# Optimization experiments

Measured on AMD Instinct MI355X. Metric: run time of the kernel, lower is better.

## Reference

```python
import jax, jax.numpy as jnp
import numpy as np
from jax import lax

# Module hyperparameters (match init_kwargs)
N_EXPERTS = 8
TOP_K = 2
N_CLUSTERS = 64
TEMP = 1.0
BETA = 0.9        # LIF membrane decay
VTH = 1.0         # LIF firing threshold
SURR_ALPHA = 4.0  # surrogate-gradient sharpness


@jax.custom_vjp
def spike(u):
    # Heaviside spike with sigmoid surrogate gradient (standard SNN practice)
    return (u >= 0).astype(u.dtype)

def _spike_fwd(u):
    return spike(u), u

def _spike_bwd(u, g):
    s = jax.nn.sigmoid(SURR_ALPHA * u)
    return (g * SURR_ALPHA * s * (1.0 - s),)

spike.defvjp(_spike_fwd, _spike_bwd)


def lif(x):
    """LIF neuron over leading time axis. x: (T, ...). Returns spikes (T, ...)."""
    def step(v, xt):
        v = BETA * v + xt
        s = spike(v - VTH)
        return v - s * VTH, s  # soft reset
    _, spikes = lax.scan(step, jnp.zeros_like(x[0]), x)
    return spikes


def setup_inputs() -> dict:
    key = jax.random.key(0)
    k1, k2, k3 = jax.random.split(key, 3)
    T, B, S, D = 4, 2, 1024, 1024
    ef = 4096 // N_EXPERTS  # 512
    x = jax.random.normal(k1, (T, B, S, D), dtype=jnp.float32)
    w_up = jax.random.normal(k2, (N_EXPERTS, D, ef), dtype=jnp.float32) / np.sqrt(D)
    w_down = jax.random.normal(k3, (N_EXPERTS, ef, D), dtype=jnp.float32) / np.sqrt(ef)
    expert_bias = jnp.zeros((N_EXPERTS,), dtype=jnp.float32)
    return {"x": x, "w_up": w_up, "w_down": w_down, "expert_bias": expert_bias}


def reference(x, w_up, w_down, expert_bias):
    T, B, S, D = x.shape
    N = B * S
    xf = x.reshape(T, N, D)

    # --- routing: LIF spikes -> cluster firing rates -> expert scores ---
    rs = lif(xf)                      # (T, N, D)
    fr = rs.mean(axis=0)              # (N, D) mean firing rate
    nc = N_CLUSTERS
    # feature d belongs to cluster d % nc -> reshape(N, D//nc, nc) sums same residues
    cr = fr.reshape(N, D // nc, nc).sum(axis=1) / (D // nc)       # (N, nc)
    cpe = nc // N_EXPERTS
    es = cr.reshape(N, N_EXPERTS, cpe).mean(axis=-1)              # (N, E)
    es = es / max(TEMP, 0.01) + expert_bias

    # --- top-k expert selection ---
    ts, ti = lax.top_k(es, TOP_K)                                 # (N, k)
    tw = jax.nn.softmax(ts, axis=-1).astype(x.dtype)              # (N, k)
    # combined per-(token, expert) weight: sum_k 1[ti==e] * tw
    w = (jax.nn.one_hot(ti, N_EXPERTS, dtype=x.dtype) * tw[..., None]).sum(axis=1)  # (N, E)

    # --- expert FFN with LIF nonlinearities (all experts, masked combine) ---
    # LIF is independent per (token, feature), so computing every expert on every
    # token and weighting by w (zero for unselected) matches the masked dispatch.
    h = jnp.einsum('tnd,edf->tenf', xf, w_up)                     # (T, E, N, ef)
    hs = lif(h)
    o = jnp.einsum('tenf,efd->tend', hs, w_down)                  # (T, E, N, D)
    os = lif(o)
    out = jnp.einsum('tend,ne->tnd', os, w).reshape(T, B, S, D)

    # --- load balance loss ---
    ef_frac = jax.nn.one_hot(ti, N_EXPERTS, dtype=jnp.float32).sum(axis=(0, 1)) / (N * TOP_K)
    rp = jax.nn.softmax(es, axis=-1).mean(axis=0)
    lb = N_EXPERTS * (ef_frac * rp).sum()
    return out, lb
```

## Files before the change

### kernel.cpp

```cpp
#include <hip/hip_runtime.h>
#include <cstdint>
#include <cstddef>

#define T_   4
#define NTOK 2048
#define D_   1024
#define EF   512
#define NE   8
#define TP   8

typedef __attribute__((ext_vector_type(4))) double d4;

#define WS_RP    0
#define WS_CNT   131072
#define WS_LTOK  131104
#define WS_LW    196640
#define WS_GMASK 327712

__global__ __launch_bounds__(256) void moe_routing(
    const float* __restrict__ x, const float* __restrict__ bias,
    double* __restrict__ rp, int* __restrict__ cnt,
    int* __restrict__ ltok, double* __restrict__ lw)
{
    const int n   = blockIdx.x;
    const int tid = threadIdx.x;
    __shared__ int scnt[NE];
    if (tid < NE) scnt[tid] = 0;
    __syncthreads();

    int c = 0;
#pragma unroll
    for (int j = 0; j < 4; ++j) {
        const int d = j * 256 + tid;
        double v = 0.0;
#pragma unroll
        for (int t = 0; t < T_; ++t) {
            v = 0.9 * v + (double)x[((size_t)t * NTOK + n) * D_ + d];
            if (v - 1.0 >= 0.0) { ++c; v -= 1.0; }
        }
    }
    c += __shfl_xor(c, 1);
    c += __shfl_xor(c, 2);
    c += __shfl_xor(c, 4);
    if ((tid & 7) == 0) atomicAdd(&scnt[(tid >> 3) & 7], c);
    __syncthreads();

    if (tid == 0) {
        double es[NE];
#pragma unroll
        for (int e = 0; e < NE; ++e)
            es[e] = (double)scnt[e] * (1.0 / 512.0) + (double)bias[e];

        int i0 = 0; double b0 = es[0];
        for (int e = 1; e < NE; ++e) if (es[e] > b0) { b0 = es[e]; i0 = e; }
        int i1 = -1; double b1 = -1e300;
        for (int e = 0; e < NE; ++e) if (e != i0 && es[e] > b1) { b1 = es[e]; i1 = e; }

        const double e1 = exp(b1 - b0);
        const double w0 = 1.0 / (1.0 + e1);
        const double w1 = e1 / (1.0 + e1);

        double mx = es[0];
        for (int e = 1; e < NE; ++e) mx = es[e] > mx ? es[e] : mx;
        double s = 0.0, ex[NE];
        for (int e = 0; e < NE; ++e) { ex[e] = exp(es[e] - mx); s += ex[e]; }
        for (int e = 0; e < NE; ++e) rp[(size_t)n * NE + e] = ex[e] / s;

        int s0 = atomicAdd(&cnt[i0], 1);
        ltok[i0 * NTOK + s0] = n; lw[i0 * NTOK + s0] = w0;
        int s1 = atomicAdd(&cnt[i1], 1);
        ltok[i1 * NTOK + s1] = n; lw[i1 * NTOK + s1] = w1;
    }
}

__global__ __launch_bounds__(256) void moe_finalize(
    const double* __restrict__ rp, const int* __restrict__ cnt,
    float* __restrict__ out_lb)
{
    __shared__ double red[256][NE];
    const int tid = threadIdx.x;
    double a[NE];
#pragma unroll
    for (int e = 0; e < NE; ++e) a[e] = 0.0;
    for (int n = tid; n < NTOK; n += 256)
#pragma unroll
        for (int e = 0; e < NE; ++e) a[e] += rp[(size_t)n * NE + e];
#pragma unroll
    for (int e = 0; e < NE; ++e) red[tid][e] = a[e];
    __syncthreads();
    if (tid < NE) {
        double s = 0.0;
        for (int i = 0; i < 256; ++i) s += red[i][tid];
        red[0][tid] = s;
    }
    __syncthreads();
    if (tid == 0) {
        double lb = 0.0;
#pragma unroll
        for (int e = 0; e < NE; ++e)
            lb += ((double)cnt[e] / (double)(NTOK * 2)) * (red[0][e] / (double)NTOK);
        out_lb[0] = (float)(8.0 * lb);
    }
}

__device__ __forceinline__ int dec_idx(double val, int* fam) {
    const double r0 = (val - 96.0) * 0.25;
    const int i0 = (int)r0;
    if ((double)i0 == r0 && i0 >= 0 && i0 < 16) { *fam = 0; return i0; }
    const double r1 = (val - 6.0) * 0.0625;
    const int i1 = (int)r1;
    if ((double)i1 == r1 && i1 >= 0 && i1 < 16) { *fam = 1; return i1; }
    *fam = -1; return 0;
}

struct Frag {
    int vA, kA, uB, kB;
    int vC[4], uC[4];
    int bad;
};

__device__ __forceinline__ Frag probe_layout(int l) {
    Frag fr; fr.bad = 0;
    const d4 zz = {0.0, 0.0, 0.0, 0.0};
    const double dl = (double)l;
    const d4 Dv = __builtin_amdgcn_mfma_f64_16x16x4f64(dl, 1.0, zz, 0, 0, 0);
    const d4 Du = __builtin_amdgcn_mfma_f64_16x16x4f64(1.0, dl, zz, 0, 0, 0);
    int famA = -1, famB = -1;
#pragma unroll
    for (int r = 0; r < 4; ++r) {
        int fa, fb;
        fr.vC[r] = dec_idx(Dv[r], &fa);
        fr.uC[r] = dec_idx(Du[r], &fb);
        if (r == 0) { famA = fa; famB = fb; }
        fr.bad |= (fa != famA) | (fb != famB) | (fa < 0) | (fb < 0);
    }
    fr.vA = (famA == 0) ? (l & 15) : (l >> 2);
    fr.kA = (famA == 0) ? (l >> 4) : (l & 3);
    fr.uB = (famB == 0) ? (l & 15) : (l >> 2);
    fr.kB = (famB == 0) ? (l >> 4) : (l & 3);
    const d4 D3 = __builtin_amdgcn_mfma_f64_16x16x4f64(
        (double)(1 << fr.kA), (double)(16 << fr.kB), zz, 0, 0, 0);
#pragma unroll
    for (int r = 0; r < 4; ++r) fr.bad |= (D3[r] != 1360.0);
    return fr;
}

__device__ __forceinline__ size_t gm_row(int e, int pairIdx, int t) {
    return ((size_t)((e << 11) + pairIdx) * 4 + t) * 32;
}

__global__ __launch_bounds__(256) void moe_up(
    const float* __restrict__ x, const float* __restrict__ wup,
    const int* __restrict__ cnt, const int* __restrict__ ltok,
    unsigned short* __restrict__ gmask)
{
    const int gid  = blockIdx.x;
    const int e    = gid & 7;
    const int tile = gid >> 3;
    const int c    = cnt[e];
    const int base = tile * TP;
    if (base >= c) return;

    const int tid = threadIdx.x;
    const int w   = tid >> 6;
    const int l   = tid & 63;

    __shared__ int    s_tok[TP];
    __shared__ double dtile[4][16][17];
    __shared__ int s_bad;

    if (tid < TP) {
        const int idx = base + tid;
        s_tok[tid] = (idx < c) ? ltok[e * NTOK + idx] : ltok[e * NTOK + base];
    }
    if (tid == 0) s_bad = 0;
    __syncthreads();

    const Frag fr = probe_layout(l);
    if (fr.bad) atomicOr(&s_bad, 1);
    __syncthreads();

    if (s_bad) {
        unsigned* gm32 = (unsigned*)gmask;
        for (int i = tid; i < TP * 4 * 16; i += 256) {
            const int pr = i >> 6;
            gm32[(gm_row(e, base + pr, (i >> 4) & 3) >> 1) + (i & 15)] = 0u;
        }
        __syncthreads();
        for (int ci = tid; ci < TP * EF; ci += 256) {
            const int pair = ci >> 9;
            const int f    = ci & (EF - 1);
            const float* wc = wup + (size_t)e * D_ * EF + f;
            const float* xb = x + (size_t)s_tok[pair] * D_;
            double hh[4] = {0.0, 0.0, 0.0, 0.0};
            for (int d = 0; d < D_; ++d) {
                const double wv = (double)wc[(size_t)d * EF];
#pragma unroll
                for (int t = 0; t < 4; ++t)
                    hh[t] = fma((double)xb[(size_t)t * NTOK * D_ + d], wv, hh[t]);
            }
            double v = 0.0;
#pragma unroll
            for (int t = 0; t < 4; ++t) {
                v = 0.9 * v + hh[t];
                if (v - 1.0 >= 0.0) {
                    v -= 1.0;
                    atomicOr(&gm32[(gm_row(e, base + pair, t) >> 1) + (f >> 5)],
                             1u << (f & 31));
                }
            }
        }
        return;
    }

    const float* xp0 = x + ((size_t)(fr.vA & 3) * NTOK + s_tok[fr.vA >> 2]) * D_ + fr.kA;
    const float* xp1 = x + ((size_t)(fr.vA & 3) * NTOK + s_tok[4 + (fr.vA >> 2)]) * D_ + fr.kA;
    const float* bp  = wup + (size_t)e * D_ * EF + (size_t)fr.kB * EF + w * 128 + fr.uB;

    const d4 zz = {0.0, 0.0, 0.0, 0.0};
    d4 acc0[8], acc1[8];
#pragma unroll
    for (int j = 0; j < 8; ++j) { acc0[j] = zz; acc1[j] = zz; }

#pragma unroll 4
    for (int kk = 0; kk < 256; ++kk) {
        const double aD0 = (double)xp0[0];
        const double aD1 = (double)xp1[0];
        float b[8];
#pragma unroll
        for (int j = 0; j < 8; ++j) b[j] = bp[j * 16];
#pragma unroll
        for (int j = 0; j < 8; ++j) {
            const double bD = (double)b[j];
            acc0[j] = __builtin_amdgcn_mfma_f64_16x16x4f64(aD0, bD, acc0[j], 0, 0, 0);
            acc1[j] = __builtin_amdgcn_mfma_f64_16x16x4f64(aD1, bD, acc1[j], 0, 0, 0);
        }
        xp0 += 4; xp1 += 4; bp += (size_t)4 * EF;
    }

    const int pp = l >> 4;
    const int cc = l & 15;
#pragma unroll
    for (int g = 0; g < 2; ++g) {
#pragma unroll
        for (int j = 0; j < 8; ++j) {
            const d4 av = g ? acc1[j] : acc0[j];
#pragma unroll
            for (int r = 0; r < 4; ++r) dtile[w][fr.vC[r]][fr.uC[r]] = av[r];
            double v = 0.0;
#pragma unroll
            for (int t = 0; t < 4; ++t) {
                v = 0.9 * v + dtile[w][pp * 4 + t][cc];
                const bool s = (v - 1.0 >= 0.0);
                if (s) v -= 1.0;
                const unsigned long long bal = __ballot(s);
                if (l < 4)
                    gmask[gm_row(e, base + g * 4 + l, t) + (w * 8 + j)] =
                        (unsigned short)(bal >> (l * 16));
            }
        }
    }
}

__global__ __launch_bounds__(256) void moe_down(
    const float* __restrict__ wdn,
    const int* __restrict__ cnt, const int* __restrict__ ltok,
    const double* __restrict__ lw, const unsigned short* __restrict__ gmask,
    float* __restrict__ out)
{
    const int gid  = blockIdx.x;
    const int e    = gid & 7;
    const int p    = (gid >> 3) & 1;
    const int tile = gid >> 4;
    const int c    = cnt[e];
    const int base = tile * TP;
    if (base >= c) return;

    const int tid = threadIdx.x;
    const int w   = tid >> 6;
    const int l   = tid & 63;

    __shared__ int    s_tok[TP];
    __shared__ double s_w[TP];
    __shared__ unsigned hm[32][17];
    __shared__ double dtile[4][16][17];
    __shared__ int s_bad;

    if (tid < TP) {
        const int idx = base + tid;
        if (idx < c) { s_tok[tid] = ltok[e * NTOK + idx]; s_w[tid] = lw[e * NTOK + idx]; }
        else         { s_tok[tid] = ltok[e * NTOK + base]; s_w[tid] = 0.0; }
    }
    if (tid == 0) s_bad = 0;
    const unsigned* gm32 = (const unsigned*)gmask;
#pragma unroll
    for (int i = tid; i < 32 * 16; i += 256) {
        const int r = i >> 4, wd = i & 15;
        hm[r][wd] = gm32[(gm_row(e, base + (r >> 2), r & 3) >> 1) + wd];
    }
    __syncthreads();

    const Frag fr = probe_layout(l);
    if (fr.bad) atomicOr(&s_bad, 1);
    __syncthreads();

    if (s_bad) {
        for (int ci = tid; ci < TP * 512; ci += 256) {
            const int pair = ci >> 9;
            const int d    = p * 512 + (ci & 511);
            const double wgt2 = s_w[pair];
            const int    nn2  = s_tok[pair];
            const float* wc = wdn + (size_t)e * EF * D_ + d;
            double o[4] = {0.0, 0.0, 0.0, 0.0};
            for (int f = 0; f < EF; ++f) {
                const double wv = (double)wc[(size_t)f * D_];
#pragma unroll
                for (int t = 0; t < 4; ++t)
                    if ((hm[pair * 4 + t][f >> 5] >> (f & 31)) & 1) o[t] += wv;
            }
            double v = 0.0;
#pragma unroll
            for (int t = 0; t < 4; ++t) {
                v = 0.9 * v + o[t];
                if (v - 1.0 >= 0.0) {
                    v -= 1.0;
                    if (wgt2 != 0.0)
                        atomicAdd(&out[((size_t)t * NTOK + nn2) * D_ + d], (float)wgt2);
                }
            }
        }
        return;
    }

    const d4 zz = {0.0, 0.0, 0.0, 0.0};
    const int pp = l >> 4;
    const int cc = l & 15;

    const float* dp = wdn + (size_t)e * EF * D_ + (size_t)fr.kB * D_
                    + p * 512 + w * 128 + fr.uB;

    d4 acc0[8], acc1[8];
#pragma unroll
    for (int j = 0; j < 8; ++j) { acc0[j] = zz; acc1[j] = zz; }

    float bC[8];
#pragma unroll
    for (int j = 0; j < 8; ++j) bC[j] = dp[j * 16];
    unsigned m0 = hm[fr.vA][0];
    unsigned m1 = hm[16 + fr.vA][0];

#pragma unroll 1
    for (int wd = 0; wd < 16; ++wd) {
        const unsigned cm0 = m0, cm1 = m1;
        const int nw = (wd < 15) ? (wd + 1) : wd;
        m0 = hm[fr.vA][nw];
        m1 = hm[16 + fr.vA][nw];
#pragma unroll
        for (int k2 = 0; k2 < 8; ++k2) {
            const bool last = (wd == 15) && (k2 == 7);
            const float* dn_ = last ? dp : (dp + (size_t)4 * D_);
            float bN[8];
#pragma unroll
            for (int j = 0; j < 8; ++j) bN[j] = dn_[j * 16];

            const int bit = k2 * 4 + fr.kA;
            const double aD0 = ((cm0 >> bit) & 1u) ? 1.0 : 0.0;
            const double aD1 = ((cm1 >> bit) & 1u) ? 1.0 : 0.0;
#pragma unroll
            for (int j = 0; j < 8; ++j) {
                const double bD = (double)bC[j];
                acc0[j] = __builtin_amdgcn_mfma_f64_16x16x4f64(aD0, bD, acc0[j], 0, 0, 0);
                acc1[j] = __builtin_amdgcn_mfma_f64_16x16x4f64(aD1, bD, acc1[j], 0, 0, 0);
            }
#pragma unroll
            for (int j = 0; j < 8; ++j) bC[j] = bN[j];
            dp = dn_;
        }
    }

#pragma unroll
    for (int g = 0; g < 2; ++g) {
        const int pair = g * 4 + pp;
        const double wgt = s_w[pair];
        const int    nn  = s_tok[pair];
#pragma unroll
        for (int j = 0; j < 8; ++j) {
            const d4 av = g ? acc1[j] : acc0[j];
#pragma unroll
            for (int r = 0; r < 4; ++r) dtile[w][fr.vC[r]][fr.uC[r]] = av[r];
            const int d = p * 512 + w * 128 + j * 16 + cc;
            double v = 0.0;
#pragma unroll
            for (int t = 0; t < 4; ++t) {
                v = 0.9 * v + dtile[w][pp * 4 + t][cc];
                if (v - 1.0 >= 0.0) {
                    v -= 1.0;
                    if (wgt != 0.0)
                        atomicAdd(&out[((size_t)t * NTOK + nn) * D_ + d], (float)wgt);
                }
            }
        }
    }
}

extern "C" void kernel_launch(void* const* d_in, const int* in_sizes, int n_in,
                              void* d_out, int out_size, void* d_ws, size_t ws_size,
                              hipStream_t stream)
{
    const float* x    = (const float*)d_in[0];
    const float* wup  = (const float*)d_in[1];
    const float* wdn  = (const float*)d_in[2];
    const float* bias = (const float*)d_in[3];
    float* out = (float*)d_out;
    char*  ws  = (char*)d_ws;

    double* rp   = (double*)(ws + WS_RP);
    int*    cnt  = (int*)(ws + WS_CNT);
    int*    ltok = (int*)(ws + WS_LTOK);
    double* lw   = (double*)(ws + WS_LW);
    unsigned short* gmask = (unsigned short*)(ws + WS_GMASK);

    hipMemsetAsync(d_out, 0, (size_t)out_size * sizeof(float), stream);
    hipMemsetAsync(cnt, 0, NE * sizeof(int), stream);

    moe_routing<<<NTOK, 256, 0, stream>>>(x, bias, rp, cnt, ltok, lw);
    moe_finalize<<<1, 256, 0, stream>>>(rp, cnt, out + (size_t)T_ * NTOK * D_);
    moe_up<<<NE * 256, 256, 0, stream>>>(x, wup, cnt, ltok, gmask);
    moe_down<<<NE * 512, 256, 0, stream>>>(wdn, cnt, ltok, lw, gmask, out);
}
```

Baseline: 798.8 us.

## Split moe_up feature dimension across two blocks and software-prefetch operands

Each moe_up block now covers half of the 512 expert features, selected by a new hf index, so twice as many blocks are launched and each holds half the accumulators. The MFMA loop also loads the next iteration's x and weight values before issuing the current MFMAs, a register-level double buffer meant to hide global-load latency. The fallback path and the gmask write offsets are adjusted to match the half split. The cost is that each x tile is now loaded twice, once per feature half.

```diff
diff --git a/kernel.cpp b/kernel.cpp
--- a/kernel.cpp
+++ b/kernel.cpp
@@ -156,7 +156,8 @@
 {
     const int gid  = blockIdx.x;
     const int e    = gid & 7;
-    const int tile = gid >> 3;
+    const int hf   = (gid >> 3) & 1;
+    const int tile = gid >> 4;
     const int c    = cnt[e];
     const int base = tile * TP;
     if (base >= c) return;
@@ -181,15 +182,15 @@
     __syncthreads();
 
     if (s_bad) {
-        unsigned* gm32 = (unsigned*)gmask;
+        unsigned short* gm16 = gmask;
         for (int i = tid; i < TP * 4 * 16; i += 256) {
             const int pr = i >> 6;
-            gm32[(gm_row(e, base + pr, (i >> 4) & 3) >> 1) + (i & 15)] = 0u;
+            gm16[gm_row(e, base + pr, (i >> 4) & 3) + hf * 16 + (i & 15)] = 0;
         }
         __syncthreads();
-        for (int ci = tid; ci < TP * EF; ci += 256) {
-            const int pair = ci >> 9;
-            const int f    = ci & (EF - 1);
+        for (int ci = tid; ci < TP * 256; ci += 256) {
+            const int pair = ci >> 8;
+            const int f    = hf * 256 + (ci & 255);
             const float* wc = wup + (size_t)e * D_ * EF + f;
             const float* xb = x + (size_t)s_tok[pair] * D_;
             double hh[4] = {0.0, 0.0, 0.0, 0.0};
@@ -205,7 +206,7 @@
                 v = 0.9 * v + hh[t];
                 if (v - 1.0 >= 0.0) {
                     v -= 1.0;
-                    atomicOr(&gm32[(gm_row(e, base + pair, t) >> 1) + (f >> 5)],
+                    atomicOr((unsigned*)&gm16[gm_row(e, base + pair, t) + (f >> 4 & ~1)],
                              1u << (f & 31));
                 }
             }
@@ -215,27 +216,42 @@
 
     const float* xp0 = x + ((size_t)(fr.vA & 3) * NTOK + s_tok[fr.vA >> 2]) * D_ + fr.kA;
     const float* xp1 = x + ((size_t)(fr.vA & 3) * NTOK + s_tok[4 + (fr.vA >> 2)]) * D_ + fr.kA;
-    const float* bp  = wup + (size_t)e * D_ * EF + (size_t)fr.kB * EF + w * 128 + fr.uB;
+    const float* bp  = wup + (size_t)e * D_ * EF + (size_t)fr.kB * EF
+                     + hf * 256 + w * 64 + fr.uB;
 
     const d4 zz = {0.0, 0.0, 0.0, 0.0};
-    d4 acc0[8], acc1[8];
-#pragma unroll
-    for (int j = 0; j < 8; ++j) { acc0[j] = zz; acc1[j] = zz; }
-
-#pragma unroll 4
+    d4 acc0[4], acc1[4];
+#pragma unroll
+    for (int j = 0; j < 4; ++j) { acc0[j] = zz; acc1[j] = zz; }
+
+    float aC0 = xp0[0], aC1 = xp1[0];
+    float bC[4];
+#pragma unroll
+    for (int j = 0; j < 4; ++j) bC[j] = bp[j * 16];
+
+#pragma unroll 2
     for (int kk = 0; kk < 256; ++kk) {
-        const double aD0 = (double)xp0[0];
-        const double aD1 = (double)xp1[0];
-        float b[8];
-#pragma unroll
-        for (int j = 0; j < 8; ++j) b[j] = bp[j * 16];
-#pragma unroll
-        for (int j = 0; j < 8; ++j) {
-            const double bD = (double)b[j];
+        const bool last = (kk == 255);
+        const float* xn0 = last ? xp0 : (xp0 + 4);
+        const float* xn1 = last ? xp1 : (xp1 + 4);
+        const float* bn  = last ? bp  : (bp + (size_t)4 * EF);
+        const float aN0 = xn0[0];
+        const float aN1 = xn1[0];
+        float bN[4];
+#pragma unroll
+        for (int j = 0; j < 4; ++j) bN[j] = bn[j * 16];
+
+        const double aD0 = (double)aC0, aD1 = (double)aC1;
+#pragma unroll
+        for (int j = 0; j < 4; ++j) {
+            const double bD = (double)bC[j];
             acc0[j] = __builtin_amdgcn_mfma_f64_16x16x4f64(aD0, bD, acc0[j], 0, 0, 0);
             acc1[j] = __builtin_amdgcn_mfma_f64_16x16x4f64(aD1, bD, acc1[j], 0, 0, 0);
         }
-        xp0 += 4; xp1 += 4; bp += (size_t)4 * EF;
+        aC0 = aN0; aC1 = aN1;
+#pragma unroll
+        for (int j = 0; j < 4; ++j) bC[j] = bN[j];
+        xp0 = xn0; xp1 = xn1; bp = bn;
     }
 
     const int pp = l >> 4;
@@ -243,7 +259,7 @@
 #pragma unroll
     for (int g = 0; g < 2; ++g) {
 #pragma unroll
-        for (int j = 0; j < 8; ++j) {
+        for (int j = 0; j < 4; ++j) {
             const d4 av = g ? acc1[j] : acc0[j];
 #pragma unroll
             for (int r = 0; r < 4; ++r) dtile[w][fr.vC[r]][fr.uC[r]] = av[r];
@@ -255,7 +271,7 @@
                 if (s) v -= 1.0;
                 const unsigned long long bal = __ballot(s);
                 if (l < 4)
-                    gmask[gm_row(e, base + g * 4 + l, t) + (w * 8 + j)] =
+                    gmask[gm_row(e, base + g * 4 + l, t) + (hf * 16 + w * 4 + j)] =
                         (unsigned short)(bal >> (l * 16));
             }
         }
@@ -425,6 +441,6 @@
 
     moe_routing<<<NTOK, 256, 0, stream>>>(x, bias, rp, cnt, ltok, lw);
     moe_finalize<<<1, 256, 0, stream>>>(rp, cnt, out + (size_t)T_ * NTOK * D_);
-    moe_up<<<NE * 256, 256, 0, stream>>>(x, wup, cnt, ltok, gmask);
+    moe_up<<<NE * 512, 256, 0, stream>>>(x, wup, cnt, ltok, gmask);
     moe_down<<<NE * 512, 256, 0, stream>>>(wdn, cnt, ltok, lw, gmask, out);
 }
```

Result: slower. 829.3 us (+3.8%).
